# Kernel optimization log

Hardware: AMD Instinct MI355X
Metric: run time of the kernel (lower is better)

## Reference

```python
import jax, jax.numpy as jnp
import numpy as np

N = 16384      # batch size
F = 1024       # n_features
H = 256        # n_dim (latent)


def setup_inputs() -> dict:
    key = jax.random.key(0)
    ks = jax.random.split(key, 6)
    X = jax.random.normal(ks[0], (N, F), dtype=jnp.float32)
    We = jax.random.normal(ks[1], (F, H), dtype=jnp.float32) / np.sqrt(F).astype(np.float32)
    be = jnp.zeros((H,), dtype=jnp.float32)
    Wd = jax.random.normal(ks[2], (H, F), dtype=jnp.float32) / np.sqrt(H).astype(np.float32)
    bd = jnp.zeros((F,), dtype=jnp.float32)
    Wc = jax.random.normal(ks[3], (H, 1), dtype=jnp.float32) / np.sqrt(H).astype(np.float32)
    bc = jnp.zeros((1,), dtype=jnp.float32)
    s = jax.random.randint(ks[4], (N,), 0, 2, dtype=jnp.int32)  # protected attribute labels in {0,1}
    return {"X": X, "We": We, "be": be, "Wd": Wd, "bd": bd, "Wc": Wc, "bc": bc, "s": s, "p": 1}


def reference(X, We, be, Wd, bd, Wc, bc, s, p):
    # encoder / decoder (single Linear each, as in the default NRL construction)
    g = X @ We + be                      # [N, H]
    rec = g @ Wd + bd                    # [N, F]
    mse_mean = jnp.mean((rec - X) ** 2)  # MSELoss is built with reduction='sum' but forward uses torch.mean(pow(...)) directly

    # critic scores for ALL rows (critics share weights: [module]*n_protected)
    c = (g @ Wc + bc)[:, 0]              # [N]

    # masked pairwise L1: sum_{i in P, j notin P} |c_i - c_j|
    mp = (s == p)                        # rows where s == p
    mpf = mp.astype(c.dtype)
    mrf = (~mp).astype(c.dtype)
    Dmat = jnp.abs(c[:, None] - c[None, :])   # [N, N] pairwise L1 (cdist equivalent)
    total = mpf @ (Dmat @ mrf)                # mp^T D mr == cdist(c_p, c_rest, p=1).sum()

    w_dist_count = mp.sum()                   # == w_dist.shape[0] (number of protected rows)
    w_dist_mean = total / w_dist_count.astype(c.dtype)

    return (mse_mean, jnp.asarray(rec.shape[0]), w_dist_mean, w_dist_count)
```

## Files before the change

kernel.cpp:

```cpp
#include <hip/hip_runtime.h>
#include <hip/hip_bf16.h>
#include <cstdint>

#define NR 16384
#define NF 1024
#define NH 256

typedef __bf16 bf16x8 __attribute__((ext_vector_type(8)));
typedef float f32x4 __attribute__((ext_vector_type(4)));
typedef unsigned short us8 __attribute__((ext_vector_type(8)));

static __device__ __forceinline__ unsigned short f2bf(float f) {
    unsigned u = __float_as_uint(f);
    u += 0x7FFFu + ((u >> 16) & 1u);
    return (unsigned short)(u >> 16);
}


__global__ __launch_bounds__(256) void prep_kernel(
    const float* __restrict__ X, const float* __restrict__ We,
    const float* __restrict__ Wd,
    unsigned short* __restrict__ Xpk, unsigned short* __restrict__ Wepk,
    unsigned short* __restrict__ Wdpk, float* __restrict__ hdr) {
    const int b = blockIdx.x, t = threadIdx.x;
    if (b == 0 && t < 160) hdr[t] = 0.f;
    if (b < 1024) {
        const int m = t & 15, k8 = t >> 4;
#pragma unroll
        for (int p = 0; p < 8; p++) {
            const int kk = k8 + 16 * p;
            const float4* xp = (const float4*)(X + (size_t)(b * 16 + m) * NF + kk * 8);
            float4 lo = xp[0], hi = xp[1];
            us8 v;
            v[0] = f2bf(lo.x); v[1] = f2bf(lo.y); v[2] = f2bf(lo.z); v[3] = f2bf(lo.w);
            v[4] = f2bf(hi.x); v[5] = f2bf(hi.y); v[6] = f2bf(hi.z); v[7] = f2bf(hi.w);
            const int kc = kk >> 2, q = kk & 3, lane = q * 16 + m;
            *(us8*)&Xpk[((size_t)(b * 32 + kc)) * 512 + lane * 8] = v;
        }
    } else if (b < 1040) {
        const int nb = b - 1024;
        const int lane = t & 63, q = lane >> 4, li = lane & 15, idx = t >> 6;
#pragma unroll
        for (int p = 0; p < 8; p++) {
            const int kc = idx + 4 * p;
            us8 v;
#pragma unroll
            for (int e = 0; e < 8; e++)
                v[e] = f2bf(We[(size_t)(kc * 32 + q * 8 + e) * NH + nb * 16 + li]);
            *(us8*)&Wepk[((size_t)(nb * 32 + kc)) * 512 + lane * 8] = v;
        }
    } else {
        const int nb4 = b - 1040;
        const int lane = t & 63, q = lane >> 4, li = lane & 15, idx = t >> 6;
#pragma unroll
        for (int p = 0; p < 8; p++) {
            const int c = nb4 * 32 + idx + 4 * p;
            const int nb = c >> 3, kc = c & 7;
            us8 v;
#pragma unroll
            for (int e = 0; e < 8; e++)
                v[e] = f2bf(Wd[(size_t)(kc * 32 + q * 8 + e) * NF + nb * 16 + li]);
            *(us8*)&Wdpk[((size_t)(nb * 8 + kc)) * 512 + lane * 8] = v;
        }
    }
}

__global__ __launch_bounds__(512) void fused_kernel(
    const float* __restrict__ X, const unsigned short* __restrict__ Xpk,
    const unsigned short* __restrict__ Wepk, const unsigned short* __restrict__ Wdpk,
    const float* __restrict__ be, const float* __restrict__ bd,
    const float* __restrict__ Wc, const int* __restrict__ s, const int* __restrict__ pv,
    float* __restrict__ cpart, float* __restrict__ hdr) {
    __shared__ unsigned short gs[64 * 256];
    __shared__ float credu[8][32];
    __shared__ float msred[8];
    const int t = threadIdx.x;
    const int mb = blockIdx.x, m0 = mb * 64;
    const int w = t >> 6, lane = t & 63, q = lane >> 4, li = lane & 15;
    const int wmh = w >> 2, wm = wmh * 32;
    const int wnq = w & 3, wn = wnq * 64;

    if (w == 0) {
        unsigned long long mbal = __ballot(s[m0 + lane] == pv[0]);
        if (lane == 0) atomicAdd((int*)(hdr + 129), (int)__popcll(mbal));
    }

    const unsigned short* Ap0 = Xpk + ((size_t)(mb * 4 + wmh * 2) * 32) * 512 + lane * 8;
    const unsigned short* Ap1 = Ap0 + (size_t)32 * 512;
    const unsigned short* Bp[4];
#pragma unroll
    for (int j = 0; j < 4; j++)
        Bp[j] = Wepk + ((size_t)(wnq * 4 + j) * 32) * 512 + lane * 8;

    f32x4 acc[2][4] = {};
#pragma unroll 2
    for (int kc = 0; kc < 32; ++kc) {
        bf16x8 af0 = __builtin_bit_cast(bf16x8, *(const us8*)(Ap0 + kc * 512));
        bf16x8 af1 = __builtin_bit_cast(bf16x8, *(const us8*)(Ap1 + kc * 512));
        bf16x8 bf[4];
#pragma unroll
        for (int j = 0; j < 4; j++)
            bf[j] = __builtin_bit_cast(bf16x8, *(const us8*)(Bp[j] + kc * 512));
#pragma unroll
        for (int j = 0; j < 4; j++) {
            acc[0][j] = __builtin_amdgcn_mfma_f32_16x16x32_bf16(bf[j], af0, acc[0][j], 0, 0, 0);
            acc[1][j] = __builtin_amdgcn_mfma_f32_16x16x32_bf16(bf[j], af1, acc[1][j], 0, 0, 0);
        }
    }

#pragma unroll
    for (int i = 0; i < 2; i++) {
        float csum = 0.f;
        const int ml = wm + i * 16 + li;
#pragma unroll
        for (int j = 0; j < 4; j++) {
            const int colb = wn + j * 16 + q * 4;
            float4 be4 = *(const float4*)&be[colb];
            float4 wc4 = *(const float4*)&Wc[colb];
            float v0 = acc[i][j][0] + be4.x;
            float v1 = acc[i][j][1] + be4.y;
            float v2 = acc[i][j][2] + be4.z;
            float v3 = acc[i][j][3] + be4.w;
            csum += v0 * wc4.x + v1 * wc4.y + v2 * wc4.z + v3 * wc4.w;
            ushort4 st = { f2bf(v0), f2bf(v1), f2bf(v2), f2bf(v3) };
            const int sl = (((wn + j * 16) >> 3) + (q >> 1)) ^ (ml & 31);
            *(ushort4*)&gs[ml * 256 + sl * 8 + (q & 1) * 4] = st;
        }
        csum += __shfl_down(csum, 32);
        csum += __shfl_down(csum, 16);
        if (lane < 16) credu[w][i * 16 + lane] = csum;
    }
    __syncthreads();
    if (t < 64) {
        const int half = t >> 5, r = t & 31;
        cpart[m0 + t] = credu[half * 4 + 0][r] + credu[half * 4 + 1][r] +
                        credu[half * 4 + 2][r] + credu[half * 4 + 3][r];
    }

    float lsum = 0.f;
#pragma unroll
    for (int pass = 0; pass < 4; ++pass) {
        const int nbase = pass * 256 + wn;
        const unsigned short* Wp[4];
#pragma unroll
        for (int j = 0; j < 4; j++)
            Wp[j] = Wdpk + ((size_t)((pass * 16 + wnq * 4 + j) * 8)) * 512 + lane * 8;
        f32x4 a2[2][4] = {};
#pragma unroll
        for (int kc = 0; kc < 8; ++kc) {
            bf16x8 af[2];
#pragma unroll
            for (int i = 0; i < 2; i++) {
                const int ml = wm + i * 16 + li;
                const int sp = (kc * 4 + q) ^ (ml & 31);
                af[i] = __builtin_bit_cast(bf16x8, *(const us8*)&gs[ml * 256 + sp * 8]);
            }
#pragma unroll
            for (int j = 0; j < 4; j++) {
                bf16x8 bf = __builtin_bit_cast(bf16x8, *(const us8*)(Wp[j] + kc * 512));
                a2[0][j] = __builtin_amdgcn_mfma_f32_16x16x32_bf16(bf, af[0], a2[0][j], 0, 0, 0);
                a2[1][j] = __builtin_amdgcn_mfma_f32_16x16x32_bf16(bf, af[1], a2[1][j], 0, 0, 0);
            }
        }
#pragma unroll
        for (int i = 0; i < 2; i++) {
            const size_t rowoff = (size_t)(m0 + wm + i * 16 + li) * NF;
#pragma unroll
            for (int j = 0; j < 4; j++) {
                const int colb = nbase + j * 16 + q * 4;
                float4 bd4 = *(const float4*)&bd[colb];
                float4 xr  = *(const float4*)&X[rowoff + colb];
                float d0 = a2[i][j][0] + bd4.x - xr.x;
                float d1 = a2[i][j][1] + bd4.y - xr.y;
                float d2 = a2[i][j][2] + bd4.z - xr.z;
                float d3 = a2[i][j][3] + bd4.w - xr.w;
                lsum += d0 * d0 + d1 * d1 + d2 * d2 + d3 * d3;
            }
        }
    }
#pragma unroll
    for (int o = 32; o; o >>= 1) lsum += __shfl_down(lsum, o);
    if (lane == 0) msred[w] = lsum;
    __syncthreads();
    if (t == 0) {
        float mm = 0.f;
#pragma unroll
        for (int ww = 0; ww < 8; ww++) mm += msred[ww];
        atomicAdd(&hdr[mb & 63], mm);
    }
}

__global__ __launch_bounds__(256) void pair_fin_kernel(
    const float* __restrict__ c, const int* __restrict__ s, const int* __restrict__ pv,
    float* __restrict__ hdr, float* __restrict__ out) {
    __shared__ float sj[1024];
    __shared__ float mj[1024];
    __shared__ float red[256];
    __shared__ int win;
    const int p = pv[0];
    const int jb = blockIdx.x * 1024;
    for (int j = threadIdx.x; j < 1024; j += 256) {
        int jj = jb + j;
        sj[j] = c[jj];
        mj[j] = (s[jj] != p) ? 1.f : 0.f;
    }
    __syncthreads();
    const int a0 = blockIdx.y * 512 + threadIdx.x, a1 = a0 + 256;
    const float ca0 = c[a0], ca1 = c[a1];
    const float f0 = (s[a0] == p) ? 1.f : 0.f;
    const float f1 = (s[a1] == p) ? 1.f : 0.f;
    float s0 = 0.f, s1 = 0.f;
#pragma unroll 8
    for (int j4 = 0; j4 < 256; j4++) {
        float4 v  = *(const float4*)&sj[j4 * 4];
        float4 m4 = *(const float4*)&mj[j4 * 4];
        s0 = fmaf(m4.x, fabsf(ca0 - v.x), s0);
        s0 = fmaf(m4.y, fabsf(ca0 - v.y), s0);
        s0 = fmaf(m4.z, fabsf(ca0 - v.z), s0);
        s0 = fmaf(m4.w, fabsf(ca0 - v.w), s0);
        s1 = fmaf(m4.x, fabsf(ca1 - v.x), s1);
        s1 = fmaf(m4.y, fabsf(ca1 - v.y), s1);
        s1 = fmaf(m4.z, fabsf(ca1 - v.z), s1);
        s1 = fmaf(m4.w, fabsf(ca1 - v.w), s1);
    }
    float sum = s0 * f0 + s1 * f1;
#pragma unroll
    for (int o = 32; o; o >>= 1) sum += __shfl_down(sum, o);
    if ((threadIdx.x & 63) == 0)
        atomicAdd(&hdr[64 + ((blockIdx.y * 16 + blockIdx.x) & 63)], sum);
    __threadfence();
    __syncthreads();
    if (threadIdx.x == 0)
        win = (atomicAdd((int*)(hdr + 128), 1) == 16 * 32 - 1) ? 1 : 0;
    __syncthreads();
    if (win) {
        float v = (threadIdx.x < 128) ? atomicAdd(&hdr[threadIdx.x], 0.f) : 0.f;
        red[threadIdx.x] = v;
        __syncthreads();
        if (threadIdx.x == 0) {
            float ms = 0.f, ps = 0.f;
            for (int i = 0; i < 64; i++) { ms += red[i]; ps += red[64 + i]; }
            int np = atomicAdd((int*)(hdr + 129), 0);
            out[0] = ms / (float)((size_t)NR * NF);
            out[1] = (float)NR;
            out[2] = ps / (float)np;
            out[3] = (float)np;
        }
    }
}

extern "C" void kernel_launch(void* const* d_in, const int* in_sizes, int n_in,
                              void* d_out, int out_size, void* d_ws, size_t ws_size,
                              hipStream_t stream) {
    const float* X  = (const float*)d_in[0];
    const float* We = (const float*)d_in[1];
    const float* be = (const float*)d_in[2];
    const float* Wd = (const float*)d_in[3];
    const float* bd = (const float*)d_in[4];
    const float* Wc = (const float*)d_in[5];
    const int*   s  = (const int*)d_in[7];
    const int*   pv = (const int*)d_in[8];

    char* ws = (char*)d_ws;
    float* hdr   = (float*)ws;
    float* cpart = (float*)(ws + 1024);
    unsigned short* Xpk  = (unsigned short*)(ws + 1024 + 65536);
    unsigned short* Wepk = Xpk + (size_t)NR * NF;
    unsigned short* Wdpk = Wepk + (size_t)NH * NF;

    prep_kernel<<<1056, 256, 0, stream>>>(X, We, Wd, Xpk, Wepk, Wdpk, hdr);
    fused_kernel<<<256, 512, 0, stream>>>(X, Xpk, Wepk, Wdpk, be, bd, Wc, s, pv, cpart, hdr);
    pair_fin_kernel<<<dim3(16, 32), 256, 0, stream>>>(cpart, s, pv, hdr, (float*)d_out);
}
```

Before: 219.4 us.

## Restructure fused autoencoder: smaller blocks, register prefetch, bf16 residual, compacted pairwise

Stages X through shared memory in the prep kernel so the global loads are coalesced when packing to bf16. The fused kernel now runs 512 blocks of 256 threads over 32 rows each and double-buffers its global fragment loads for both GEMMs. The MSE residual reads the packed bf16 X instead of the fp32 original, which cuts memory traffic but adds bf16 rounding to the loss. A new compaction kernel splits critic scores into protected and rest arrays so the pairwise kernel skips the mask multiplies and any empty tiles.

New measurement: 198.0 us. -9.7%, faster.

```diff
diff --git a/kernel.cpp b/kernel.cpp
--- a/kernel.cpp
+++ b/kernel.cpp
@@ -14,6 +14,9 @@
     unsigned u = __float_as_uint(f);
     u += 0x7FFFu + ((u >> 16) & 1u);
     return (unsigned short)(u >> 16);
+}
+static __device__ __forceinline__ float bf2f(unsigned short h) {
+    return __uint_as_float(((unsigned)h) << 16);
 }
 
 
@@ -23,19 +26,33 @@
     unsigned short* __restrict__ Xpk, unsigned short* __restrict__ Wepk,
     unsigned short* __restrict__ Wdpk, float* __restrict__ hdr) {
     const int b = blockIdx.x, t = threadIdx.x;
-    if (b == 0 && t < 160) hdr[t] = 0.f;
+    if (b == 0 && t < 192) hdr[t] = 0.f;
     if (b < 1024) {
-        const int m = t & 15, k8 = t >> 4;
-#pragma unroll
-        for (int p = 0; p < 8; p++) {
-            const int kk = k8 + 16 * p;
-            const float4* xp = (const float4*)(X + (size_t)(b * 16 + m) * NF + kk * 8);
-            float4 lo = xp[0], hi = xp[1];
-            us8 v;
-            v[0] = f2bf(lo.x); v[1] = f2bf(lo.y); v[2] = f2bf(lo.z); v[3] = f2bf(lo.w);
-            v[4] = f2bf(hi.x); v[5] = f2bf(hi.y); v[6] = f2bf(hi.z); v[7] = f2bf(hi.w);
-            const int kc = kk >> 2, q = kk & 3, lane = q * 16 + m;
-            *(us8*)&Xpk[((size_t)(b * 32 + kc)) * 512 + lane * 8] = v;
+        __shared__ float tile[16 * 272];
+        const int r0 = b * 16;
+#pragma unroll
+        for (int ch = 0; ch < 4; ++ch) {
+            const int c0 = ch * 256;
+#pragma unroll
+            for (int p = 0; p < 4; ++p) {
+                int idx = t + 256 * p;
+                int r = idx >> 6, c4 = idx & 63;
+                *(float4*)&tile[r * 272 + c4 * 4] =
+                    *(const float4*)(X + (size_t)(r0 + r) * NF + c0 + c4 * 4);
+            }
+            __syncthreads();
+#pragma unroll
+            for (int p = 0; p < 2; ++p) {
+                int u = t + 256 * p;
+                int cell = u >> 6, lane = u & 63;
+                int m = lane & 15, q = lane >> 4;
+                const float* src = &tile[m * 272 + cell * 32 + q * 8];
+                us8 v;
+#pragma unroll
+                for (int e = 0; e < 8; e++) v[e] = f2bf(src[e]);
+                *(us8*)&Xpk[((size_t)(b * 32 + ch * 8 + cell)) * 512 + lane * 8] = v;
+            }
+            __syncthreads();
         }
     } else if (b < 1040) {
         const int nb = b - 1024;
@@ -65,53 +82,66 @@
     }
 }
 
-__global__ __launch_bounds__(512) void fused_kernel(
-    const float* __restrict__ X, const unsigned short* __restrict__ Xpk,
+__global__ __launch_bounds__(256) void fused_kernel(
+    const unsigned short* __restrict__ Xpk,
     const unsigned short* __restrict__ Wepk, const unsigned short* __restrict__ Wdpk,
     const float* __restrict__ be, const float* __restrict__ bd,
-    const float* __restrict__ Wc, const int* __restrict__ s, const int* __restrict__ pv,
+    const float* __restrict__ Wc,
     float* __restrict__ cpart, float* __restrict__ hdr) {
-    __shared__ unsigned short gs[64 * 256];
-    __shared__ float credu[8][32];
-    __shared__ float msred[8];
+    __shared__ unsigned short gs[32 * 256];
+    __shared__ float credu[4][32];
+    __shared__ float msred[4];
     const int t = threadIdx.x;
-    const int mb = blockIdx.x, m0 = mb * 64;
+    const int b = blockIdx.x, m0 = b * 32;
     const int w = t >> 6, lane = t & 63, q = lane >> 4, li = lane & 15;
-    const int wmh = w >> 2, wm = wmh * 32;
-    const int wnq = w & 3, wn = wnq * 64;
-
-    if (w == 0) {
-        unsigned long long mbal = __ballot(s[m0 + lane] == pv[0]);
-        if (lane == 0) atomicAdd((int*)(hdr + 129), (int)__popcll(mbal));
-    }
-
-    const unsigned short* Ap0 = Xpk + ((size_t)(mb * 4 + wmh * 2) * 32) * 512 + lane * 8;
+    const int wn = w * 64;
+
+    const unsigned short* Ap0 = Xpk + ((size_t)(b * 2) * 32) * 512 + lane * 8;
     const unsigned short* Ap1 = Ap0 + (size_t)32 * 512;
     const unsigned short* Bp[4];
 #pragma unroll
     for (int j = 0; j < 4; j++)
-        Bp[j] = Wepk + ((size_t)(wnq * 4 + j) * 32) * 512 + lane * 8;
-
+        Bp[j] = Wepk + ((size_t)(w * 4 + j) * 32) * 512 + lane * 8;
+
+    us8 fa[2][2], fb[2][4];
+#pragma unroll
+    for (int z = 0; z < 2; ++z) {
+        fa[z][0] = *(const us8*)(Ap0 + z * 512);
+        fa[z][1] = *(const us8*)(Ap1 + z * 512);
+#pragma unroll
+        for (int j = 0; j < 4; j++) fb[z][j] = *(const us8*)(Bp[j] + z * 512);
+    }
     f32x4 acc[2][4] = {};
-#pragma unroll 2
+#pragma unroll
     for (int kc = 0; kc < 32; ++kc) {
-        bf16x8 af0 = __builtin_bit_cast(bf16x8, *(const us8*)(Ap0 + kc * 512));
-        bf16x8 af1 = __builtin_bit_cast(bf16x8, *(const us8*)(Ap1 + kc * 512));
-        bf16x8 bf[4];
-#pragma unroll
-        for (int j = 0; j < 4; j++)
-            bf[j] = __builtin_bit_cast(bf16x8, *(const us8*)(Bp[j] + kc * 512));
+        const int cb = kc & 1;
+        us8 na0, na1, nbv[4];
+        const bool pf = (kc + 2 < 32);
+        if (pf) {
+            na0 = *(const us8*)(Ap0 + (kc + 2) * 512);
+            na1 = *(const us8*)(Ap1 + (kc + 2) * 512);
+#pragma unroll
+            for (int j = 0; j < 4; j++) nbv[j] = *(const us8*)(Bp[j] + (kc + 2) * 512);
+        }
+        bf16x8 a0 = __builtin_bit_cast(bf16x8, fa[cb][0]);
+        bf16x8 a1 = __builtin_bit_cast(bf16x8, fa[cb][1]);
 #pragma unroll
         for (int j = 0; j < 4; j++) {
-            acc[0][j] = __builtin_amdgcn_mfma_f32_16x16x32_bf16(bf[j], af0, acc[0][j], 0, 0, 0);
-            acc[1][j] = __builtin_amdgcn_mfma_f32_16x16x32_bf16(bf[j], af1, acc[1][j], 0, 0, 0);
+            bf16x8 bf = __builtin_bit_cast(bf16x8, fb[cb][j]);
+            acc[0][j] = __builtin_amdgcn_mfma_f32_16x16x32_bf16(bf, a0, acc[0][j], 0, 0, 0);
+            acc[1][j] = __builtin_amdgcn_mfma_f32_16x16x32_bf16(bf, a1, acc[1][j], 0, 0, 0);
+        }
+        if (pf) {
+            fa[cb][0] = na0; fa[cb][1] = na1;
+#pragma unroll
+            for (int j = 0; j < 4; j++) fb[cb][j] = nbv[j];
         }
     }
 
 #pragma unroll
     for (int i = 0; i < 2; i++) {
         float csum = 0.f;
-        const int ml = wm + i * 16 + li;
+        const int ml = i * 16 + li;
 #pragma unroll
         for (int j = 0; j < 4; j++) {
             const int colb = wn + j * 16 + q * 4;
@@ -123,58 +153,74 @@
             float v3 = acc[i][j][3] + be4.w;
             csum += v0 * wc4.x + v1 * wc4.y + v2 * wc4.z + v3 * wc4.w;
             ushort4 st = { f2bf(v0), f2bf(v1), f2bf(v2), f2bf(v3) };
-            const int sl = (((wn + j * 16) >> 3) + (q >> 1)) ^ (ml & 31);
-            *(ushort4*)&gs[ml * 256 + sl * 8 + (q & 1) * 4] = st;
+            const int phys = ((colb >> 3)) ^ ml;
+            *(ushort4*)&gs[ml * 256 + phys * 8 + (q & 1) * 4] = st;
         }
         csum += __shfl_down(csum, 32);
         csum += __shfl_down(csum, 16);
         if (lane < 16) credu[w][i * 16 + lane] = csum;
     }
     __syncthreads();
-    if (t < 64) {
-        const int half = t >> 5, r = t & 31;
-        cpart[m0 + t] = credu[half * 4 + 0][r] + credu[half * 4 + 1][r] +
-                        credu[half * 4 + 2][r] + credu[half * 4 + 3][r];
-    }
+    if (t < 32)
+        cpart[m0 + t] = credu[0][t] + credu[1][t] + credu[2][t] + credu[3][t];
+
+    const unsigned short* Wp = Wdpk + lane * 8;
+    us8 gb[2][4];
+#pragma unroll
+    for (int z = 0; z < 2; ++z)
+#pragma unroll
+        for (int j = 0; j < 4; j++)
+            gb[z][j] = *(const us8*)(Wp + ((size_t)((w * 4 + j) * 8 + z)) * 512);
 
     float lsum = 0.f;
-#pragma unroll
-    for (int pass = 0; pass < 4; ++pass) {
-        const int nbase = pass * 256 + wn;
-        const unsigned short* Wp[4];
-#pragma unroll
-        for (int j = 0; j < 4; j++)
-            Wp[j] = Wdpk + ((size_t)((pass * 16 + wnq * 4 + j) * 8)) * 512 + lane * 8;
-        f32x4 a2[2][4] = {};
-#pragma unroll
-        for (int kc = 0; kc < 8; ++kc) {
-            bf16x8 af[2];
+    f32x4 a2[2][4] = {};
+#pragma unroll
+    for (int it = 0; it < 32; ++it) {
+        const int cb = it & 1, pass = it >> 3, kc = it & 7;
+        us8 nbv[4];
+        const bool pf = (it + 2 < 32);
+        if (pf) {
+            const int p2 = (it + 2) >> 3, k2 = (it + 2) & 7;
+#pragma unroll
+            for (int j = 0; j < 4; j++)
+                nbv[j] = *(const us8*)(Wp + ((size_t)((p2 * 16 + w * 4 + j) * 8 + k2)) * 512);
+        }
+        bf16x8 af[2];
+#pragma unroll
+        for (int i = 0; i < 2; i++) {
+            const int ml = i * 16 + li;
+            const int phys = (kc * 4 + q) ^ ml;
+            af[i] = __builtin_bit_cast(bf16x8, *(const us8*)&gs[ml * 256 + phys * 8]);
+        }
+#pragma unroll
+        for (int j = 0; j < 4; j++) {
+            bf16x8 bf = __builtin_bit_cast(bf16x8, gb[cb][j]);
+            a2[0][j] = __builtin_amdgcn_mfma_f32_16x16x32_bf16(bf, af[0], a2[0][j], 0, 0, 0);
+            a2[1][j] = __builtin_amdgcn_mfma_f32_16x16x32_bf16(bf, af[1], a2[1][j], 0, 0, 0);
+        }
+        if (pf) {
+#pragma unroll
+            for (int j = 0; j < 4; j++) gb[cb][j] = nbv[j];
+        }
+        if (kc == 7) {
 #pragma unroll
             for (int i = 0; i < 2; i++) {
-                const int ml = wm + i * 16 + li;
-                const int sp = (kc * 4 + q) ^ (ml & 31);
-                af[i] = __builtin_bit_cast(bf16x8, *(const us8*)&gs[ml * 256 + sp * 8]);
-            }
-#pragma unroll
-            for (int j = 0; j < 4; j++) {
-                bf16x8 bf = __builtin_bit_cast(bf16x8, *(const us8*)(Wp[j] + kc * 512));
-                a2[0][j] = __builtin_amdgcn_mfma_f32_16x16x32_bf16(bf, af[0], a2[0][j], 0, 0, 0);
-                a2[1][j] = __builtin_amdgcn_mfma_f32_16x16x32_bf16(bf, af[1], a2[1][j], 0, 0, 0);
-            }
-        }
-#pragma unroll
-        for (int i = 0; i < 2; i++) {
-            const size_t rowoff = (size_t)(m0 + wm + i * 16 + li) * NF;
-#pragma unroll
-            for (int j = 0; j < 4; j++) {
-                const int colb = nbase + j * 16 + q * 4;
-                float4 bd4 = *(const float4*)&bd[colb];
-                float4 xr  = *(const float4*)&X[rowoff + colb];
-                float d0 = a2[i][j][0] + bd4.x - xr.x;
-                float d1 = a2[i][j][1] + bd4.y - xr.y;
-                float d2 = a2[i][j][2] + bd4.z - xr.z;
-                float d3 = a2[i][j][3] + bd4.w - xr.w;
-                lsum += d0 * d0 + d1 * d1 + d2 * d2 + d3 * d3;
+                const int mbp = b * 2 + i;
+#pragma unroll
+                for (int j = 0; j < 4; j++) {
+                    const int colb = pass * 256 + wn + j * 16 + q * 4;
+                    float4 bd4 = *(const float4*)&bd[colb];
+                    const int kcx = pass * 8 + w * 2 + (j >> 1);
+                    const int qp = (j & 1) * 2 + (q >> 1), h = q & 1;
+                    ushort4 xv = *(const ushort4*)&Xpk[((size_t)(mbp * 32 + kcx)) * 512 +
+                                                       (qp * 16 + li) * 8 + h * 4];
+                    float d0 = a2[i][j][0] + bd4.x - bf2f(xv.x);
+                    float d1 = a2[i][j][1] + bd4.y - bf2f(xv.y);
+                    float d2 = a2[i][j][2] + bd4.z - bf2f(xv.z);
+                    float d3 = a2[i][j][3] + bd4.w - bf2f(xv.w);
+                    lsum += d0 * d0 + d1 * d1 + d2 * d2 + d3 * d3;
+                    a2[i][j] = (f32x4){0.f, 0.f, 0.f, 0.f};
+                }
             }
         }
     }
@@ -182,52 +228,73 @@
     for (int o = 32; o; o >>= 1) lsum += __shfl_down(lsum, o);
     if (lane == 0) msred[w] = lsum;
     __syncthreads();
-    if (t == 0) {
-        float mm = 0.f;
-#pragma unroll
-        for (int ww = 0; ww < 8; ww++) mm += msred[ww];
-        atomicAdd(&hdr[mb & 63], mm);
+    if (t == 0)
+        atomicAdd(&hdr[b & 63], msred[0] + msred[1] + msred[2] + msred[3]);
+}
+
+__global__ __launch_bounds__(256) void compact_kernel(
+    const float* __restrict__ c, const int* __restrict__ s, const int* __restrict__ pv,
+    float* __restrict__ cP, float* __restrict__ cR, int* __restrict__ cnt) {
+    int i = blockIdx.x * 256 + threadIdx.x;
+    float ci = c[i];
+    bool pr = (s[i] == pv[0]);
+    int lane = threadIdx.x & 63;
+    unsigned long long m = __ballot(pr);
+    {
+        int cm = __popcll(m);
+        int base = 0;
+        if (lane == 0 && cm) base = atomicAdd(&cnt[0], cm);
+        base = __shfl(base, 0);
+        int off = __popcll(m & ((1ull << lane) - 1ull));
+        if (pr) cP[base + off] = ci;
+    }
+    {
+        unsigned long long mm = ~m;
+        int cm = __popcll(mm);
+        int base = 0;
+        if (lane == 0 && cm) base = atomicAdd(&cnt[1], cm);
+        base = __shfl(base, 0);
+        int off = __popcll(mm & ((1ull << lane) - 1ull));
+        if (!pr) cR[base + off] = ci;
     }
 }
 
 __global__ __launch_bounds__(256) void pair_fin_kernel(
-    const float* __restrict__ c, const int* __restrict__ s, const int* __restrict__ pv,
+    const float* __restrict__ cP, const float* __restrict__ cR,
     float* __restrict__ hdr, float* __restrict__ out) {
     __shared__ float sj[1024];
-    __shared__ float mj[1024];
     __shared__ float red[256];
     __shared__ int win;
-    const int p = pv[0];
+    const int nP = ((const int*)hdr)[129];
+    const int nR = ((const int*)hdr)[130];
     const int jb = blockIdx.x * 1024;
-    for (int j = threadIdx.x; j < 1024; j += 256) {
-        int jj = jb + j;
-        sj[j] = c[jj];
-        mj[j] = (s[jj] != p) ? 1.f : 0.f;
-    }
-    __syncthreads();
-    const int a0 = blockIdx.y * 512 + threadIdx.x, a1 = a0 + 256;
-    const float ca0 = c[a0], ca1 = c[a1];
-    const float f0 = (s[a0] == p) ? 1.f : 0.f;
-    const float f1 = (s[a1] == p) ? 1.f : 0.f;
-    float s0 = 0.f, s1 = 0.f;
+    int jn = nR - jb; if (jn < 0) jn = 0; if (jn > 1024) jn = 1024;
+    float sum = 0.f;
+    if (jn > 0 && blockIdx.y * 512 < nP) {
+        for (int j = threadIdx.x; j < 1024; j += 256)
+            sj[j] = (jb + j < nR) ? cR[jb + j] : 0.f;
+        __syncthreads();
+        const int a0 = blockIdx.y * 512 + threadIdx.x, a1 = a0 + 256;
+        const float ca0 = (a0 < nP) ? cP[a0] : 0.f;
+        const float ca1 = (a1 < nP) ? cP[a1] : 0.f;
+        float s0 = 0.f, s1 = 0.f;
 #pragma unroll 8
-    for (int j4 = 0; j4 < 256; j4++) {
-        float4 v  = *(const float4*)&sj[j4 * 4];
-        float4 m4 = *(const float4*)&mj[j4 * 4];
-        s0 = fmaf(m4.x, fabsf(ca0 - v.x), s0);
-        s0 = fmaf(m4.y, fabsf(ca0 - v.y), s0);
-        s0 = fmaf(m4.z, fabsf(ca0 - v.z), s0);
-        s0 = fmaf(m4.w, fabsf(ca0 - v.w), s0);
-        s1 = fmaf(m4.x, fabsf(ca1 - v.x), s1);
-        s1 = fmaf(m4.y, fabsf(ca1 - v.y), s1);
-        s1 = fmaf(m4.z, fabsf(ca1 - v.z), s1);
-        s1 = fmaf(m4.w, fabsf(ca1 - v.w), s1);
-    }
-    float sum = s0 * f0 + s1 * f1;
-#pragma unroll
-    for (int o = 32; o; o >>= 1) sum += __shfl_down(sum, o);
-    if ((threadIdx.x & 63) == 0)
-        atomicAdd(&hdr[64 + ((blockIdx.y * 16 + blockIdx.x) & 63)], sum);
+        for (int j4 = 0; j4 < 256; j4++) {
+            float4 v = *(const float4*)&sj[j4 * 4];
+            s0 += fabsf(ca0 - v.x) + fabsf(ca0 - v.y) + fabsf(ca0 - v.z) + fabsf(ca0 - v.w);
+            s1 += fabsf(ca1 - v.x) + fabsf(ca1 - v.y) + fabsf(ca1 - v.z) + fabsf(ca1 - v.w);
+        }
+        float pad = (float)(1024 - jn);
+        s0 -= pad * fabsf(ca0);
+        s1 -= pad * fabsf(ca1);
+        if (a0 >= nP) s0 = 0.f;
+        if (a1 >= nP) s1 = 0.f;
+        sum = s0 + s1;
+#pragma unroll
+        for (int o = 32; o; o >>= 1) sum += __shfl_down(sum, o);
+        if ((threadIdx.x & 63) == 0 && sum != 0.f)
+            atomicAdd(&hdr[64 + ((blockIdx.y * 16 + blockIdx.x) & 63)], sum);
+    }
     __threadfence();
     __syncthreads();
     if (threadIdx.x == 0)
@@ -264,11 +331,14 @@
     char* ws = (char*)d_ws;
     float* hdr   = (float*)ws;
     float* cpart = (float*)(ws + 1024);
-    unsigned short* Xpk  = (unsigned short*)(ws + 1024 + 65536);
+    float* cP    = (float*)(ws + 1024 + 65536);
+    float* cR    = (float*)(ws + 1024 + 2 * 65536);
+    unsigned short* Xpk  = (unsigned short*)(ws + 1024 + 3 * 65536);
     unsigned short* Wepk = Xpk + (size_t)NR * NF;
     unsigned short* Wdpk = Wepk + (size_t)NH * NF;
 
     prep_kernel<<<1056, 256, 0, stream>>>(X, We, Wd, Xpk, Wepk, Wdpk, hdr);
-    fused_kernel<<<256, 512, 0, stream>>>(X, Xpk, Wepk, Wdpk, be, bd, Wc, s, pv, cpart, hdr);
-    pair_fin_kernel<<<dim3(16, 32), 256, 0, stream>>>(cpart, s, pv, hdr, (float*)d_out);
-}
+    fused_kernel<<<512, 256, 0, stream>>>(Xpk, Wepk, Wdpk, be, bd, Wc, cpart, hdr);
+    compact_kernel<<<64, 256, 0, stream>>>(cpart, s, pv, cP, cR, (int*)hdr + 129);
+    pair_fin_kernel<<<dim3(16, 32), 256, 0, stream>>>(cP, cR, hdr, (float*)d_out);
+}
```
